# Kernel optimization log

Measured on AMD Instinct MI355X. Metric: run time of the kernel, lower is better.

## Reference

```python
import jax, jax.numpy as jnp
import numpy as np

HIDDEN = 768
KV_DIM = HIDDEN // 3  # 256
BATCH, SEQ = 2, 8192
THETA = 10000.0


def rope_table(seq_len, dim):
    # Matches LlamaRotaryEmbedding: returns [1, seq_len, dim] sinusoid table
    pos = jnp.arange(seq_len, dtype=jnp.float32)                       # [S]
    freqs = THETA ** (-jnp.arange(0, dim, 2, dtype=jnp.float32) / dim)  # [dim/2]
    ang = pos[:, None] * freqs[None, :]                                 # [S, dim/2]
    return jnp.concatenate([jnp.sin(ang), jnp.cos(ang)], axis=-1)[None]  # [1, S, dim]


def setup_inputs() -> dict:
    key = jax.random.key(0)
    kx, kq, kk, kv, ko = jax.random.split(key, 5)
    s = 1.0 / np.sqrt(HIDDEN)
    return {
        "x": jax.random.normal(kx, (BATCH, SEQ, HIDDEN), dtype=jnp.float32),
        # torch nn.Linear weights: [out_features, in_features], y = x @ W.T
        "Wq": jax.random.uniform(kq, (HIDDEN, HIDDEN), jnp.float32, -s, s),
        "Wk": jax.random.uniform(kk, (KV_DIM, HIDDEN), jnp.float32, -s, s),
        "Wv": jax.random.uniform(kv, (KV_DIM, HIDDEN), jnp.float32, -s, s),
        "Wo": jax.random.uniform(ko, (HIDDEN, KV_DIM), jnp.float32, -s, s),
    }


def reference(x, Wq, Wk, Wv, Wo):
    B, S, H = x.shape
    # q/k projections are computed in the original but immediately OVERWRITTEN
    # by the rope table (the rope module ignores its input values). Kept here
    # for faithfulness; XLA will DCE them in forward.
    q = jnp.einsum('bsh,oh->bso', x, Wq)
    k = jnp.einsum('bsh,oh->bso', x, Wk)
    v = jnp.einsum('bsh,oh->bso', x, Wv)                # [B, S, KV_DIM]
    r = rope_table(S, H)                                 # [1, S, H] -> q == k == r
    attn_weights = jnp.matmul(r, jnp.swapaxes(r, -2, -1))  # [1, S, S]
    attn_probs = jax.nn.softmax(attn_weights, axis=-1)      # [1, S, S]
    attn_output = jnp.matmul(attn_probs, v)                 # broadcast -> [B, S, KV_DIM]
    out = jnp.einsum('bsk,ok->bso', attn_output, Wo)        # [B, S, H]
    return out
```

## Files before the change

### kernel.cpp

```cpp
#include <hip/hip_runtime.h>


typedef unsigned short u16;
typedef __attribute__((ext_vector_type(8))) short short8;
typedef __attribute__((ext_vector_type(8))) _Float16 f16x8;
typedef __attribute__((ext_vector_type(4))) float float4v;

__device__ inline u16 f16b(float f) {
  union { _Float16 h; u16 u; } v; v.h = (_Float16)f; return v.u;
}

__device__ inline u16 f32_to_bf16(float f) {
  union { float f; unsigned int u; } v; v.f = f;
  unsigned int r = v.u + 0x7FFF + ((v.u >> 16) & 1);
  return (u16)(r >> 16);
}

__device__ inline void gld_lds16(const u16* g, u16* l) {
  auto gp = (const __attribute__((address_space(1))) unsigned int*)(g);
  auto lp = (__attribute__((address_space(3))) unsigned int*)(l);
  __builtin_amdgcn_global_load_lds(gp, lp, 16, 0, 0);
}

__device__ inline int swzkey(int r) { return ((r >> 1) ^ (r >> 3)) & 3; }

__global__ __launch_bounds__(256)
void prep_w(const float* __restrict__ Wv, const float* __restrict__ Wo,
            u16* __restrict__ wt) {
  __shared__ __align__(16) float wo[4][256];
  const int og = blockIdx.x / 3, hc = blockIdx.x % 3;
  const int o0 = og * 4;
  ((float4v*)&wo[0][0])[threadIdx.x] =
      ((const float4v*)(Wo + (size_t)o0 * 256))[threadIdx.x];
  __syncthreads();
  const int h = hc * 256 + threadIdx.x;
  float acc[4] = {0.f, 0.f, 0.f, 0.f};
  for (int k = 0; k < 256; k += 8) {
    float wv[8];
#pragma unroll
    for (int u = 0; u < 8; ++u) wv[u] = Wv[(size_t)(k + u) * 768 + h];
#pragma unroll
    for (int j = 0; j < 4; ++j) {
      float4v c0 = *(const float4v*)(&wo[j][k]);
      float4v c1 = *(const float4v*)(&wo[j][k + 4]);
      acc[j] = fmaf(c0[0], wv[0], acc[j]);
      acc[j] = fmaf(c0[1], wv[1], acc[j]);
      acc[j] = fmaf(c0[2], wv[2], acc[j]);
      acc[j] = fmaf(c0[3], wv[3], acc[j]);
      acc[j] = fmaf(c1[0], wv[4], acc[j]);
      acc[j] = fmaf(c1[1], wv[5], acc[j]);
      acc[j] = fmaf(c1[2], wv[6], acc[j]);
      acc[j] = fmaf(c1[3], wv[7], acc[j]);
    }
  }
  const int kt = h >> 5, c = (h >> 3) & 3, kr = h & 7;
#pragma unroll
  for (int j = 0; j < 4; ++j) {
    const int o = o0 + j;
    wt[((size_t)(kt * 768 + o)) * 32 + ((c ^ swzkey(o)) << 3) + kr] =
        f16b(acc[j]);
  }
}

__global__ __launch_bounds__(256, 3)
void gemm_xw(const float* __restrict__ x, const u16* __restrict__ wt,
             float* __restrict__ out) {
  __shared__ __align__(16) u16 As[2][128 * 32];
  __shared__ __align__(16) u16 Bs[3][128 * 32];

  const int tid = threadIdx.x;
  const int w = tid >> 6, l = tid & 63;
  const int q = l >> 4, mr = l & 15;
  const int wm = w & 1, wn = w >> 1;

  const int sb = (blockIdx.x & 7) * 96 + (blockIdx.x >> 3);
  const int mt = sb / 6, nt = sb - mt * 6;
  const int row0 = mt * 128, col0 = nt * 128;

  const int ar = tid >> 1, ac = (tid & 1) << 4;
  const float* xg = x + (size_t)(row0 + ar) * 768 + ac;
  const int fa = swzkey(ar);
  const int aw0 = ar * 32 + ((((ac >> 3) + 0) ^ fa) << 3);
  const int aw1 = ar * 32 + ((((ac >> 3) + 1) ^ fa) << 3);
  const u16* wtb = wt + (size_t)col0 * 32 + tid * 8;

  int avo[4], bvo[4];
#pragma unroll
  for (int i = 0; i < 4; ++i) {
    const int r = wm * 64 + i * 16 + mr;
    avo[i] = r * 32 + ((q ^ swzkey(r)) << 3);
    const int o = wn * 64 + i * 16 + mr;
    bvo[i] = o * 32 + ((q ^ swzkey(o)) << 3);
  }

  float4v acc[4][4];
#pragma unroll
  for (int i = 0; i < 4; ++i)
#pragma unroll
    for (int j = 0; j < 4; ++j) acc[i][j] = (float4v){0.f, 0.f, 0.f, 0.f};

  float4v eA0, eA1, eA2, eA3;
  float4v oA0, oA1, oA2, oA3;

#define ISSUE_B(slot, tile)                                                  \
  { const u16* g = wtb + (size_t)(tile) * 24576;                             \
    gld_lds16(g,        &Bs[slot][tid * 8]);                                 \
    gld_lds16(g + 2048, &Bs[slot][2048 + tid * 8]); }

#define ISSUE_A(r0_, r1_, r2_, r3_, tile)                                    \
  { const float* xk = xg + (size_t)(tile) * 32;                              \
    r0_ = *(const float4v*)(xk);      r1_ = *(const float4v*)(xk + 4);       \
    r2_ = *(const float4v*)(xk + 8);  r3_ = *(const float4v*)(xk + 12); }

#define CVT_A(r0_, r1_, r2_, r3_, slot)                                      \
  { union { u16 h[8]; short8 s; } p0, p1;                                    \
    _Pragma("unroll")                                                        \
    for (int e = 0; e < 4; ++e) {                                            \
      p0.h[e] = f16b(r0_[e]); p0.h[e + 4] = f16b(r1_[e]);                    \
      p1.h[e] = f16b(r2_[e]); p1.h[e + 4] = f16b(r3_[e]);                    \
    }                                                                        \
    *(short8*)(&As[slot][aw0]) = p0.s;                                       \
    *(short8*)(&As[slot][aw1]) = p1.s; }

#define MFMA_STEP(aslot, bbase)                                              \
  { const u16* Ab = &As[aslot][0];                                           \
    const u16* Bb = (bbase);                                                 \
    f16x8 av[4], bv[4];                                                      \
    _Pragma("unroll")                                                        \
    for (int i = 0; i < 4; ++i) av[i] = *(const f16x8*)(&Ab[avo[i]]);        \
    _Pragma("unroll")                                                        \
    for (int j = 0; j < 4; ++j) bv[j] = *(const f16x8*)(&Bb[bvo[j]]);        \
    __builtin_amdgcn_s_setprio(1);                                           \
    _Pragma("unroll")                                                        \
    for (int i = 0; i < 4; ++i)                                              \
      _Pragma("unroll")                                                      \
      for (int j = 0; j < 4; ++j)                                            \
        acc[i][j] = __builtin_amdgcn_mfma_f32_16x16x32_f16(av[i], bv[j], acc[i][j], 0, 0, 0); \
    __builtin_amdgcn_s_setprio(0); }

  ISSUE_B(0, 0);
  ISSUE_A(eA0, eA1, eA2, eA3, 0);
  asm volatile("" ::: "memory");
  ISSUE_B(1, 1);
  ISSUE_A(oA0, oA1, oA2, oA3, 1);
  asm volatile("s_waitcnt vmcnt(6)" ::: "memory");
  CVT_A(eA0, eA1, eA2, eA3, 0);
  asm volatile("s_waitcnt lgkmcnt(0)" ::: "memory");
  __builtin_amdgcn_s_barrier();

  int b0 = 0, b1 = 1, b2 = 2;
  for (int p = 0; p < 11; ++p) {
    const int t = 2 * p;
    ISSUE_B(b2, t + 2);
    ISSUE_A(eA0, eA1, eA2, eA3, t + 2);
    asm volatile("s_waitcnt vmcnt(6)" ::: "memory");
    CVT_A(oA0, oA1, oA2, oA3, 1);
    MFMA_STEP(0, &Bs[b0][0]);
    asm volatile("s_waitcnt lgkmcnt(0)" ::: "memory");
    __builtin_amdgcn_s_barrier();
    ISSUE_B(b0, t + 3);
    ISSUE_A(oA0, oA1, oA2, oA3, t + 3);
    asm volatile("s_waitcnt vmcnt(6)" ::: "memory");
    CVT_A(eA0, eA1, eA2, eA3, 0);
    MFMA_STEP(1, &Bs[b1][0]);
    asm volatile("s_waitcnt lgkmcnt(0)" ::: "memory");
    __builtin_amdgcn_s_barrier();
    const int n0 = b2, n1 = b0, n2 = b1;
    b0 = n0; b1 = n1; b2 = n2;
  }

  asm volatile("s_waitcnt vmcnt(0)" ::: "memory");
  CVT_A(oA0, oA1, oA2, oA3, 1);
  MFMA_STEP(0, &Bs[b0][0]);
  asm volatile("s_waitcnt lgkmcnt(0)" ::: "memory");
  __builtin_amdgcn_s_barrier();
  MFMA_STEP(1, &Bs[b1][0]);

#undef ISSUE_B
#undef ISSUE_A
#undef CVT_A
#undef MFMA_STEP

#pragma unroll
  for (int i = 0; i < 4; ++i)
#pragma unroll
    for (int j = 0; j < 4; ++j) {
      const int r0 = row0 + wm * 64 + i * 16 + q * 4;
      const int c  = col0 + wn * 64 + j * 16 + mr;
#pragma unroll
      for (int r = 0; r < 4; ++r)
        out[(size_t)(r0 + r) * 768 + c] = acc[i][j][r];
    }
}

__global__ __launch_bounds__(512, 1)
void fused_fallback(const float* __restrict__ x,
                    const float* __restrict__ Wv, const float* __restrict__ Wo,
                    float* __restrict__ out) {
  __shared__ __align__(16) u16 As[64 * 32];
  __shared__ __align__(16) u16 Bs[256 * 32];
  __shared__ __align__(16) u16 Vs[64 * 264];

  const int tid = threadIdx.x;
  const int w  = tid >> 6, l = tid & 63;
  const int q  = l >> 4, mr = l & 15;
  const int wm = w & 1, wn = w >> 1;
  const int row0 = blockIdx.x * 64;
  const int xr = tid >> 3, xg = (tid & 7) * 4;
  const int wr = tid >> 1, wh = (tid & 1) * 16;

  float4v acc[2][4];
#pragma unroll
  for (int i = 0; i < 2; ++i)
#pragma unroll
    for (int j = 0; j < 4; ++j) acc[i][j] = (float4v){0.f, 0.f, 0.f, 0.f};

  for (int kt = 0; kt < 24; ++kt) {
    const int k0 = kt * 32;
    {
      float4v v = *(const float4v*)(x + (size_t)(row0 + xr) * 768 + k0 + xg);
      union { u16 h[4]; uint2 u; } p;
      p.h[0] = f32_to_bf16(v[0]); p.h[1] = f32_to_bf16(v[1]);
      p.h[2] = f32_to_bf16(v[2]); p.h[3] = f32_to_bf16(v[3]);
      *(uint2*)(As + xr * 32 + xg) = p.u;
    }
    {
      const float* g = Wv + (size_t)wr * 768 + k0 + wh;
      union { u16 h[16]; short8 s[2]; } p;
#pragma unroll
      for (int u = 0; u < 4; ++u) {
        float4v v = *(const float4v*)(g + u * 4);
        p.h[u * 4 + 0] = f32_to_bf16(v[0]); p.h[u * 4 + 1] = f32_to_bf16(v[1]);
        p.h[u * 4 + 2] = f32_to_bf16(v[2]); p.h[u * 4 + 3] = f32_to_bf16(v[3]);
      }
      *(short8*)(Bs + wr * 32 + wh) = p.s[0];
      *(short8*)(Bs + wr * 32 + wh + 8) = p.s[1];
    }
    __syncthreads();

    short8 a[2], b[4];
#pragma unroll
    for (int i = 0; i < 2; ++i)
      a[i] = *(const short8*)(As + (wm * 32 + i * 16 + mr) * 32 + q * 8);
#pragma unroll
    for (int j = 0; j < 4; ++j)
      b[j] = *(const short8*)(Bs + (wn * 64 + j * 16 + mr) * 32 + q * 8);
#pragma unroll
    for (int i = 0; i < 2; ++i)
#pragma unroll
      for (int j = 0; j < 4; ++j)
        acc[i][j] = __builtin_amdgcn_mfma_f32_16x16x32_bf16(a[i], b[j], acc[i][j], 0, 0, 0);
    __syncthreads();
  }

#pragma unroll
  for (int i = 0; i < 2; ++i)
#pragma unroll
    for (int j = 0; j < 4; ++j) {
      int row = wm * 32 + i * 16 + q * 4;
      int col = wn * 64 + j * 16 + mr;
#pragma unroll
      for (int r = 0; r < 4; ++r)
        Vs[(row + r) * 264 + col] = f32_to_bf16(acc[i][j][r]);
    }
  __syncthreads();

  for (int c = 0; c < 3; ++c) {
    float4v acc2[2][4];
#pragma unroll
    for (int i = 0; i < 2; ++i)
#pragma unroll
      for (int j = 0; j < 4; ++j) acc2[i][j] = (float4v){0.f, 0.f, 0.f, 0.f};

    for (int kt = 0; kt < 8; ++kt) {
      const int k0 = kt * 32;
      {
        const float* g = Wo + (size_t)(c * 256 + wr) * 256 + k0 + wh;
        union { u16 h[16]; short8 s[2]; } p;
#pragma unroll
        for (int u = 0; u < 4; ++u) {
          float4v v = *(const float4v*)(g + u * 4);
          p.h[u * 4 + 0] = f32_to_bf16(v[0]); p.h[u * 4 + 1] = f32_to_bf16(v[1]);
          p.h[u * 4 + 2] = f32_to_bf16(v[2]); p.h[u * 4 + 3] = f32_to_bf16(v[3]);
        }
        *(short8*)(Bs + wr * 32 + wh) = p.s[0];
        *(short8*)(Bs + wr * 32 + wh + 8) = p.s[1];
      }
      __syncthreads();

      short8 a[2], b[4];
#pragma unroll
      for (int i = 0; i < 2; ++i)
        a[i] = *(const short8*)(Vs + (wm * 32 + i * 16 + mr) * 264 + k0 + q * 8);
#pragma unroll
      for (int j = 0; j < 4; ++j)
        b[j] = *(const short8*)(Bs + (wn * 64 + j * 16 + mr) * 32 + q * 8);
#pragma unroll
      for (int i = 0; i < 2; ++i)
#pragma unroll
        for (int j = 0; j < 4; ++j)
          acc2[i][j] = __builtin_amdgcn_mfma_f32_16x16x32_bf16(a[i], b[j], acc2[i][j], 0, 0, 0);
      __syncthreads();
    }

#pragma unroll
    for (int i = 0; i < 2; ++i)
#pragma unroll
      for (int j = 0; j < 4; ++j) {
        int row = row0 + wm * 32 + i * 16 + q * 4;
        int col = c * 256 + wn * 64 + j * 16 + mr;
#pragma unroll
        for (int r = 0; r < 4; ++r)
          out[(size_t)(row + r) * 768 + col] = acc2[i][j][r];
      }
  }
}

extern "C" void kernel_launch(void* const* d_in, const int* in_sizes, int n_in,
                              void* d_out, int out_size, void* d_ws, size_t ws_size,
                              hipStream_t stream) {
  (void)in_sizes; (void)n_in; (void)out_size;
  const float* x  = (const float*)d_in[0];
  const float* Wv = (const float*)d_in[3];
  const float* Wo = (const float*)d_in[4];
  float* out = (float*)d_out;

  if (ws_size >= (size_t)768 * 768 * 2) {
    u16* wt = (u16*)d_ws;
    prep_w<<<dim3(576), dim3(256), 0, stream>>>(Wv, Wo, wt);
    gemm_xw<<<dim3(768), dim3(256), 0, stream>>>(x, wt, out);
  } else {
    fused_fallback<<<dim3(256), dim3(512), 0, stream>>>(x, Wv, Wo, out);
  }
}
```

Before: 149.1 us.

## Enlarge GEMM tile to 256x256 with 8 waves and phased ping-pong pipeline

The x@W GEMM moves from 128x128 tiles with 4 waves to 256x256 tiles with 8 waves, a K-step of 64, and one 128KB LDS buffer split into double-buffered A and B halves. The prepped weight layout is changed to match, with an XOR swizzle over 8 chunks. The main loop is split into quarter-tile phases that interleave global loads, fp16 conversion and MFMAs, with two barriers per phase. The aim is to raise arithmetic intensity and cut global traffic per FLOP. In exchange, only 192 blocks are launched, which may underfill the 256 CUs, and the extra barriers plus higher register pressure can hurt.

```diff
diff --git a/kernel.cpp b/kernel.cpp
--- a/kernel.cpp
+++ b/kernel.cpp
@@ -21,8 +21,6 @@
   auto lp = (__attribute__((address_space(3))) unsigned int*)(l);
   __builtin_amdgcn_global_load_lds(gp, lp, 16, 0, 0);
 }
-
-__device__ inline int swzkey(int r) { return ((r >> 1) ^ (r >> 3)) & 3; }
 
 __global__ __launch_bounds__(256)
 void prep_w(const float* __restrict__ Wv, const float* __restrict__ Wo,
@@ -53,144 +51,158 @@
       acc[j] = fmaf(c1[3], wv[7], acc[j]);
     }
   }
-  const int kt = h >> 5, c = (h >> 3) & 3, kr = h & 7;
+  const int kt = h >> 6, c6 = (h >> 3) & 7, e = h & 7;
 #pragma unroll
   for (int j = 0; j < 4; ++j) {
     const int o = o0 + j;
-    wt[((size_t)(kt * 768 + o)) * 32 + ((c ^ swzkey(o)) << 3) + kr] =
-        f16b(acc[j]);
-  }
-}
-
-__global__ __launch_bounds__(256, 3)
+    const int nto = o >> 8, half = (o >> 7) & 1, col = o & 127;
+    wt[((((size_t)(nto * 12 + kt) * 2 + half) * 128 + col) * 8 +
+        (c6 ^ (col & 7))) * 8 + e] = f16b(acc[j]);
+  }
+}
+
+__global__ __launch_bounds__(512, 2)
 void gemm_xw(const float* __restrict__ x, const u16* __restrict__ wt,
              float* __restrict__ out) {
-  __shared__ __align__(16) u16 As[2][128 * 32];
-  __shared__ __align__(16) u16 Bs[3][128 * 32];
+  __shared__ __align__(16) u16 S[65536];
 
   const int tid = threadIdx.x;
   const int w = tid >> 6, l = tid & 63;
   const int q = l >> 4, mr = l & 15;
   const int wm = w & 1, wn = w >> 1;
 
-  const int sb = (blockIdx.x & 7) * 96 + (blockIdx.x >> 3);
-  const int mt = sb / 6, nt = sb - mt * 6;
-  const int row0 = mt * 128, col0 = nt * 128;
-
-  const int ar = tid >> 1, ac = (tid & 1) << 4;
-  const float* xg = x + (size_t)(row0 + ar) * 768 + ac;
-  const int fa = swzkey(ar);
-  const int aw0 = ar * 32 + ((((ac >> 3) + 0) ^ fa) << 3);
-  const int aw1 = ar * 32 + ((((ac >> 3) + 1) ^ fa) << 3);
-  const u16* wtb = wt + (size_t)col0 * 32 + tid * 8;
-
-  int avo[4], bvo[4];
-#pragma unroll
-  for (int i = 0; i < 4; ++i) {
-    const int r = wm * 64 + i * 16 + mr;
-    avo[i] = r * 32 + ((q ^ swzkey(r)) << 3);
-    const int o = wn * 64 + i * 16 + mr;
-    bvo[i] = o * 32 + ((q ^ swzkey(o)) << 3);
-  }
-
-  float4v acc[4][4];
-#pragma unroll
-  for (int i = 0; i < 4; ++i)
+  const int sb = (blockIdx.x & 7) * 24 + (blockIdx.x >> 3);
+  const int mt = sb / 3, nt = sb - mt * 3;
+  const int row0 = mt * 256, col0 = nt * 256;
+
+  const int arow = tid >> 2, t2 = (tid & 3) << 1;
+  const float* xg = x + (size_t)(row0 + arow) * 768 + (t2 << 3);
+  const int akey = arow & 7;
+  const int aw0 = arow * 64 + (((t2    ) ^ akey) << 3);
+  const int aw1 = arow * 64 + (((t2 + 1) ^ akey) << 3);
+
+  const u16* wtb = wt + (size_t)nt * 196608 + tid * 8;
+
+  const int lkey = mr & 7;
+  const u16* Ab0 = S + (wm * 64 + mr) * 64 + (((q    ) ^ lkey) << 3);
+  const u16* Ab1 = S + (wm * 64 + mr) * 64 + (((4 + q) ^ lkey) << 3);
+  const u16* Bb0 = S + 32768 + (wn * 32 + mr) * 64 + (((q    ) ^ lkey) << 3);
+  const u16* Bb1 = S + 32768 + (wn * 32 + mr) * 64 + (((4 + q) ^ lkey) << 3);
+
+  float4v acc[8][4];
+#pragma unroll
+  for (int i = 0; i < 8; ++i)
 #pragma unroll
     for (int j = 0; j < 4; ++j) acc[i][j] = (float4v){0.f, 0.f, 0.f, 0.f};
 
-  float4v eA0, eA1, eA2, eA3;
-  float4v oA0, oA1, oA2, oA3;
-
-#define ISSUE_B(slot, tile)                                                  \
-  { const u16* g = wtb + (size_t)(tile) * 24576;                             \
-    gld_lds16(g,        &Bs[slot][tid * 8]);                                 \
-    gld_lds16(g + 2048, &Bs[slot][2048 + tid * 8]); }
-
-#define ISSUE_A(r0_, r1_, r2_, r3_, tile)                                    \
-  { const float* xk = xg + (size_t)(tile) * 32;                              \
-    r0_ = *(const float4v*)(xk);      r1_ = *(const float4v*)(xk + 4);       \
-    r2_ = *(const float4v*)(xk + 8);  r3_ = *(const float4v*)(xk + 12); }
-
-#define CVT_A(r0_, r1_, r2_, r3_, slot)                                      \
-  { union { u16 h[8]; short8 s; } p0, p1;                                    \
+  float4v ae0, ae1, ae2, ae3;
+  float4v ao0, ao1, ao2, ao3;
+
+#define ISSUE_A(r0_, r1_, r2_, r3_, T, h)                                    \
+  { const float* p = xg + (size_t)(h) * 98304 + (size_t)(T) * 64;            \
+    r0_ = *(const float4v*)(p);      r1_ = *(const float4v*)(p + 4);         \
+    r2_ = *(const float4v*)(p + 8);  r3_ = *(const float4v*)(p + 12); }
+
+#define CVT_A(r0_, r1_, r2_, r3_, cbuf, h)                                   \
+  { union { u16 hh[8]; short8 s8; } p0, p1;                                  \
     _Pragma("unroll")                                                        \
     for (int e = 0; e < 4; ++e) {                                            \
-      p0.h[e] = f16b(r0_[e]); p0.h[e + 4] = f16b(r1_[e]);                    \
-      p1.h[e] = f16b(r2_[e]); p1.h[e + 4] = f16b(r3_[e]);                    \
+      p0.hh[e] = f16b(r0_[e]); p0.hh[e + 4] = f16b(r1_[e]);                  \
+      p1.hh[e] = f16b(r2_[e]); p1.hh[e + 4] = f16b(r3_[e]);                  \
     }                                                                        \
-    *(short8*)(&As[slot][aw0]) = p0.s;                                       \
-    *(short8*)(&As[slot][aw1]) = p1.s; }
-
-#define MFMA_STEP(aslot, bbase)                                              \
-  { const u16* Ab = &As[aslot][0];                                           \
-    const u16* Bb = (bbase);                                                 \
-    f16x8 av[4], bv[4];                                                      \
+    u16* d = S + (cbuf) * 16384 + (h) * 8192;                                \
+    *(short8*)(d + aw0) = p0.s8;                                             \
+    *(short8*)(d + aw1) = p1.s8; }
+
+#define ISSUE_B(T, h)                                                        \
+  { const u16* g = wtb + (size_t)(T) * 16384 + (h) * 8192;                   \
+    u16* d = S + 32768 + ((T) & 1) * 16384 + (h) * 8192 + tid * 8;           \
+    gld_lds16(g, d); gld_lds16(g + 4096, d + 4096); }
+
+#define PHASE(cbuf, S_, U_, STAGE, WAITN, CVT)                               \
+  { f16x8 av[4][2], bv[2][2];                                                \
     _Pragma("unroll")                                                        \
-    for (int i = 0; i < 4; ++i) av[i] = *(const f16x8*)(&Ab[avo[i]]);        \
+    for (int im = 0; im < 4; ++im) {                                         \
+      av[im][0] = *(const f16x8*)(Ab0 + (cbuf) * 16384 + ((S_) * 128 + im * 16) * 64); \
+      av[im][1] = *(const f16x8*)(Ab1 + (cbuf) * 16384 + ((S_) * 128 + im * 16) * 64); \
+    }                                                                        \
     _Pragma("unroll")                                                        \
-    for (int j = 0; j < 4; ++j) bv[j] = *(const f16x8*)(&Bb[bvo[j]]);        \
+    for (int jn = 0; jn < 2; ++jn) {                                         \
+      bv[jn][0] = *(const f16x8*)(Bb0 + (cbuf) * 16384 + ((U_) * 128 + jn * 16) * 64); \
+      bv[jn][1] = *(const f16x8*)(Bb1 + (cbuf) * 16384 + ((U_) * 128 + jn * 16) * 64); \
+    }                                                                        \
+    STAGE;                                                                   \
+    asm volatile("s_waitcnt vmcnt(" #WAITN ")" ::: "memory");                \
+    CVT;                                                                     \
+    asm volatile("s_waitcnt lgkmcnt(0)" ::: "memory");                       \
+    __builtin_amdgcn_s_barrier();                                            \
     __builtin_amdgcn_s_setprio(1);                                           \
     _Pragma("unroll")                                                        \
-    for (int i = 0; i < 4; ++i)                                              \
+    for (int kk = 0; kk < 2; ++kk)                                           \
       _Pragma("unroll")                                                      \
-      for (int j = 0; j < 4; ++j)                                            \
-        acc[i][j] = __builtin_amdgcn_mfma_f32_16x16x32_f16(av[i], bv[j], acc[i][j], 0, 0, 0); \
-    __builtin_amdgcn_s_setprio(0); }
-
+      for (int im = 0; im < 4; ++im)                                         \
+        _Pragma("unroll")                                                    \
+        for (int jn = 0; jn < 2; ++jn)                                       \
+          acc[(S_) * 4 + im][(U_) * 2 + jn] = __builtin_amdgcn_mfma_f32_16x16x32_f16( \
+              av[im][kk], bv[jn][kk], acc[(S_) * 4 + im][(U_) * 2 + jn], 0, 0, 0); \
+    __builtin_amdgcn_s_setprio(0);                                           \
+    __builtin_amdgcn_s_barrier(); }
+
+  ISSUE_A(ae0, ae1, ae2, ae3, 0, 0);
   ISSUE_B(0, 0);
-  ISSUE_A(eA0, eA1, eA2, eA3, 0);
-  asm volatile("" ::: "memory");
-  ISSUE_B(1, 1);
-  ISSUE_A(oA0, oA1, oA2, oA3, 1);
+  ISSUE_A(ao0, ao1, ao2, ao3, 0, 1);
+  ISSUE_B(0, 1);
+  asm volatile("s_waitcnt vmcnt(8)" ::: "memory");
+  CVT_A(ae0, ae1, ae2, ae3, 0, 0);
   asm volatile("s_waitcnt vmcnt(6)" ::: "memory");
-  CVT_A(eA0, eA1, eA2, eA3, 0);
   asm volatile("s_waitcnt lgkmcnt(0)" ::: "memory");
   __builtin_amdgcn_s_barrier();
 
-  int b0 = 0, b1 = 1, b2 = 2;
-  for (int p = 0; p < 11; ++p) {
-    const int t = 2 * p;
-    ISSUE_B(b2, t + 2);
-    ISSUE_A(eA0, eA1, eA2, eA3, t + 2);
-    asm volatile("s_waitcnt vmcnt(6)" ::: "memory");
-    CVT_A(oA0, oA1, oA2, oA3, 1);
-    MFMA_STEP(0, &Bs[b0][0]);
-    asm volatile("s_waitcnt lgkmcnt(0)" ::: "memory");
-    __builtin_amdgcn_s_barrier();
-    ISSUE_B(b0, t + 3);
-    ISSUE_A(oA0, oA1, oA2, oA3, t + 3);
-    asm volatile("s_waitcnt vmcnt(6)" ::: "memory");
-    CVT_A(eA0, eA1, eA2, eA3, 0);
-    MFMA_STEP(1, &Bs[b1][0]);
-    asm volatile("s_waitcnt lgkmcnt(0)" ::: "memory");
-    __builtin_amdgcn_s_barrier();
-    const int n0 = b2, n1 = b0, n2 = b1;
-    b0 = n0; b1 = n1; b2 = n2;
-  }
-
-  asm volatile("s_waitcnt vmcnt(0)" ::: "memory");
-  CVT_A(oA0, oA1, oA2, oA3, 1);
-  MFMA_STEP(0, &Bs[b0][0]);
-  asm volatile("s_waitcnt lgkmcnt(0)" ::: "memory");
-  __builtin_amdgcn_s_barrier();
-  MFMA_STEP(1, &Bs[b1][0]);
-
-#undef ISSUE_B
+  for (int t = 0; t < 10; t += 2) {
+    PHASE(0, 0, 0, ISSUE_A(ae0, ae1, ae2, ae3, t + 1, 0), 6,
+          CVT_A(ao0, ao1, ao2, ao3, 0, 1))
+    PHASE(0, 1, 0, ISSUE_B(t + 1, 0), 6, )
+    PHASE(0, 0, 1, ISSUE_A(ao0, ao1, ao2, ao3, t + 1, 1), 6,
+          CVT_A(ae0, ae1, ae2, ae3, 1, 0))
+    PHASE(0, 1, 1, ISSUE_B(t + 1, 1), 6, )
+    PHASE(1, 0, 0, ISSUE_A(ae0, ae1, ae2, ae3, t + 2, 0), 6,
+          CVT_A(ao0, ao1, ao2, ao3, 1, 1))
+    PHASE(1, 1, 0, ISSUE_B(t + 2, 0), 6, )
+    PHASE(1, 0, 1, ISSUE_A(ao0, ao1, ao2, ao3, t + 2, 1), 6,
+          CVT_A(ae0, ae1, ae2, ae3, 0, 0))
+    PHASE(1, 1, 1, ISSUE_B(t + 2, 1), 6, )
+  }
+
+  PHASE(0, 0, 0, ISSUE_A(ae0, ae1, ae2, ae3, 11, 0), 6,
+        CVT_A(ao0, ao1, ao2, ao3, 0, 1))
+  PHASE(0, 1, 0, ISSUE_B(11, 0), 6, )
+  PHASE(0, 0, 1, ISSUE_A(ao0, ao1, ao2, ao3, 11, 1), 6,
+        CVT_A(ae0, ae1, ae2, ae3, 1, 0))
+  PHASE(0, 1, 1, ISSUE_B(11, 1), 6, )
+  PHASE(1, 0, 0, , 2, CVT_A(ao0, ao1, ao2, ao3, 1, 1))
+  PHASE(1, 1, 0, , 2, )
+  PHASE(1, 0, 1, , 0, )
+  PHASE(1, 1, 1, , 0, )
+
 #undef ISSUE_A
 #undef CVT_A
-#undef MFMA_STEP
-
-#pragma unroll
-  for (int i = 0; i < 4; ++i)
-#pragma unroll
-    for (int j = 0; j < 4; ++j) {
-      const int r0 = row0 + wm * 64 + i * 16 + q * 4;
-      const int c  = col0 + wn * 64 + j * 16 + mr;
-#pragma unroll
-      for (int r = 0; r < 4; ++r)
-        out[(size_t)(r0 + r) * 768 + c] = acc[i][j][r];
-    }
+#undef ISSUE_B
+#undef PHASE
+
+#pragma unroll
+  for (int s = 0; s < 2; ++s)
+#pragma unroll
+    for (int im = 0; im < 4; ++im)
+#pragma unroll
+      for (int u = 0; u < 2; ++u)
+#pragma unroll
+        for (int jn = 0; jn < 2; ++jn) {
+          const int r0 = row0 + s * 128 + wm * 64 + im * 16 + q * 4;
+          const int c  = col0 + u * 128 + wn * 32 + jn * 16 + mr;
+#pragma unroll
+          for (int r = 0; r < 4; ++r)
+            out[(size_t)(r0 + r) * 768 + c] = acc[s * 4 + im][u * 2 + jn][r];
+        }
 }
 
 __global__ __launch_bounds__(512, 1)
@@ -328,7 +340,7 @@
   if (ws_size >= (size_t)768 * 768 * 2) {
     u16* wt = (u16*)d_ws;
     prep_w<<<dim3(576), dim3(256), 0, stream>>>(Wv, Wo, wt);
-    gemm_xw<<<dim3(768), dim3(256), 0, stream>>>(x, wt, out);
+    gemm_xw<<<dim3(192), dim3(512), 0, stream>>>(x, wt, out);
   } else {
     fused_fallback<<<dim3(256), dim3(512), 0, stream>>>(x, Wv, Wo, out);
   }
```

Result: no change. 150.0 us (+0.6%).
